# Kernel optimization log

Hardware: AMD Instinct MI355X
Metric: run time of the kernel (lower is better)

Reference implementation:

```python
import jax, jax.numpy as jnp
import numpy as np

B, N, D, H = 4, 2048, 256, 4
DH = D // H          # 64
SCALE = DH ** (-0.5)
LN_EPS = 1e-5


def setup_inputs() -> dict:
    key = jax.random.key(0)
    ks = jax.random.split(key, 16)
    g = lambda k, shape, fan_in: jax.random.normal(k, shape, jnp.float32) / np.sqrt(fan_in)
    # Weights stored as [in, out] (pre-transposed vs torch Linear)
    return {
        "x0": jax.random.normal(ks[0], (B, N, D), jnp.float32),
        "x1": jax.random.normal(ks[1], (B, N, D), jnp.float32),
        "Wqk": g(ks[2], (D, D), D), "bqk": jnp.zeros((D,), jnp.float32),
        "Wv": g(ks[3], (D, D), D), "bv": jnp.zeros((D,), jnp.float32),
        "Wout": g(ks[4], (D, D), D), "bout": jnp.zeros((D,), jnp.float32),
        "Wf1": g(ks[5], (2 * D, 2 * D), 2 * D), "bf1": jnp.zeros((2 * D,), jnp.float32),
        "ln_g": jnp.ones((2 * D,), jnp.float32), "ln_b": jnp.zeros((2 * D,), jnp.float32),
        "Wf2": g(ks[6], (2 * D, D), 2 * D), "bf2": jnp.zeros((D,), jnp.float32),
    }


def _split_heads(t):
    # [B,N,D] -> [B,H,N,DH]
    b, n, _ = t.shape
    return t.reshape(b, n, H, DH).transpose(0, 2, 1, 3)


def _merge_heads(t):
    # [B,H,N,DH] -> [B,N,D]
    b, h, n, dh = t.shape
    return t.transpose(0, 2, 1, 3).reshape(b, n, h * dh)


def _layernorm(x, g, b):
    mu = jnp.mean(x, axis=-1, keepdims=True)
    var = jnp.mean(jnp.square(x - mu), axis=-1, keepdims=True)
    return (x - mu) * jax.lax.rsqrt(var + LN_EPS) * g + b


def reference(x0, x1, Wqk, bqk, Wv, bv, Wout, bout, Wf1, bf1, ln_g, ln_b, Wf2, bf2):
    qk0 = _split_heads(x0 @ Wqk + bqk)   # [B,H,N,DH]
    qk1 = _split_heads(x1 @ Wqk + bqk)
    v0 = _split_heads(x0 @ Wv + bv)
    v1 = _split_heads(x1 @ Wv + bv)

    ss = SCALE ** 0.5
    sim = jnp.einsum('bhid,bhjd->bhij', qk0 * ss, qk1 * ss)  # shared score matrix
    attn01 = jax.nn.softmax(sim, axis=-1)   # normalize over j
    attn10 = jax.nn.softmax(sim, axis=-2)   # normalize over i (== softmax(sim^T) transposed)
    m0 = jnp.einsum('bhij,bhjd->bhid', attn01, v1)
    m1 = jnp.einsum('bhji,bhjd->bhid', attn10, v0)

    m0 = _merge_heads(m0) @ Wout + bout   # [B,N,D]
    m1 = _merge_heads(m1) @ Wout + bout

    def ffn(x):
        h = x @ Wf1 + bf1                 # [B,N,2D]
        h = jax.nn.gelu(_layernorm(h, ln_g, ln_b), approximate=False)
        return h @ Wf2 + bf2              # [B,N,D]

    y0 = x0 + ffn(jnp.concatenate([x0, m0], axis=-1))
    y1 = x1 + ffn(jnp.concatenate([x1, m1], axis=-1))
    return (y0, y1)
```

## Files before the change

kernel.cpp:

```cpp
#include <hip/hip_runtime.h>
#include <hip/hip_bf16.h>
#include <math.h>

typedef __bf16 bf16;
typedef __attribute__((ext_vector_type(8))) __bf16 bf16x8;
typedef __attribute__((ext_vector_type(4))) __bf16 bf16x4;
typedef __attribute__((ext_vector_type(2))) __bf16 bf16x2;
typedef __attribute__((ext_vector_type(4))) float f32x4;
typedef __attribute__((ext_vector_type(16))) float f32x16;
typedef __attribute__((ext_vector_type(4))) unsigned u32x4;

#define MFMA(a,b,c)   __builtin_amdgcn_mfma_f32_16x16x32_bf16(a,b,c,0,0,0)
#define MFMA32(a,b,c) __builtin_amdgcn_mfma_f32_32x32x16_bf16(a,b,c,0,0,0)

static constexpr int Bb = 4, Nn = 2048, Hh = 4;
static constexpr float SS2 = 0.4246609001440095f;

__device__ __forceinline__ void lds16(const bf16* src, bf16* dst) {
  __builtin_amdgcn_global_load_lds(
      (const __attribute__((address_space(1))) void*)src,
      (__attribute__((address_space(3))) void*)dst, 16, 0, 0);
}

__device__ __forceinline__ f32x16 zero16() {
  f32x16 t;
#pragma unroll
  for (int i = 0; i < 16; ++i) t[i] = 0.f;
  return t;
}

__global__ __launch_bounds__(256) void prep_k(
    const float* Wqk, const float* Wv, const float* Wout, const float* bout,
    const float* Wf1, const float* Wf2, const float* x0, const float* x1,
    bf16* wqkv_t, bf16* wout_b, bf16* wfold_t, bf16* wf1b_t, bf16* wf2_t,
    bf16* xb0, bf16* xb1) {
  int id = blockIdx.x * 256 + threadIdx.x;
  if (id < 65536) { int k = id >> 8, n = id & 255; wqkv_t[n*256 + k] = (bf16)Wqk[id]; return; }
  id -= 65536;
  if (id < 65536) { int k = id >> 8, n = id & 255; wqkv_t[(256 + n)*256 + k] = (bf16)Wv[id]; return; }
  id -= 65536;
  if (id < 98304) {
    if (id < 65536) { wout_b[id] = (bf16)Wout[id]; }
    else { int id3 = id - 65536; int r = id3 >> 8, k = id3 & 255;
           wout_b[(256 + r)*256 + k] = (r == 0) ? (bf16)bout[k] : (bf16)0.f; }
    return; }
  id -= 98304;
  if (id < 131072) { int o = id & 511, k = id >> 9; wfold_t[o*512 + k] = (bf16)Wf1[k*512 + o]; return; }
  id -= 131072;
  if (id < 131072) { int o = id & 511, k = id >> 9; wf1b_t[o*256 + k] = (bf16)Wf1[(256 + k)*512 + o]; return; }
  id -= 131072;
  if (id < 131072) { int k = id >> 8, n = id & 255; wf2_t[n*512 + k] = (bf16)Wf2[id]; return; }
  id -= 131072;
  if (id < 1048576) {
    const float* xs = (id < 524288) ? x0 : x1;
    bf16* xd = (id < 524288) ? xb0 : xb1;
    int j = (id < 524288) ? id : id - 524288;
    f32x4 v = *reinterpret_cast<const f32x4*>(&xs[(size_t)j * 4]);
    bf16x4 o; o[0] = (bf16)v[0]; o[1] = (bf16)v[1]; o[2] = (bf16)v[2]; o[3] = (bf16)v[3];
    *reinterpret_cast<bf16x4*>(&xd[(size_t)j * 4]) = o;
  }
}

__global__ __launch_bounds__(256, 2) void qkvfold_k(
    const bf16* xb0, const bf16* xb1, const bf16* wqkv_t,
    const float* bqk, const float* bv,
    bf16* qks0, bf16* qks1, bf16* vT0, bf16* vT1,
    const bf16* wout_b, const bf16* wf1b_t, const float* bf1,
    bf16* wfold_t, float* bfold) {
  const int fid = blockIdx.x;
  const bool fold = fid >= 512;
  int bx, by, bz;
  if (!fold) {
    bx = ((fid & 7) << 3) + ((fid >> 3) & 7);
    by = (fid >> 6) & 3;
    bz = fid >> 8;
  } else {
    int id = fid - 512;
    bx = id % 3; by = id / 3; bz = 0;
  }

  const bf16* Aa = fold ? wout_b : (bz ? xb1 : xb0);
  const bf16* Wt = fold ? wf1b_t : wqkv_t;

  const int tid = threadIdx.x;
  const int lane = tid & 63;
  const int w = tid >> 6;
  const int wr = w >> 1, wc = w & 1;
  const int m0r = bx * 128;
  const int n0 = by * 128;
  const int r15 = lane & 15, g = lane >> 4, rb = r15 & 7;
  const int l3 = lane >> 3, l7 = lane & 7;
  const int swzc = (l7 ^ l3) * 8;

  __shared__ bf16 At[2][8192];
  __shared__ bf16 Bt[2][8192];

  const bf16* aA = Aa + (size_t)(m0r + w*32 + l3) * 256 + swzc;
  const bf16* bB = Wt + (size_t)(n0 + w*32 + l3) * 256 + swzc;
  const int adst = (w*32) * 64;

  auto stage = [&](int buf, int kc) {
#pragma unroll
    for (int i = 0; i < 4; i++)
      lds16(aA + kc*64 + (size_t)i * 8 * 256, &At[buf][adst + i*512]);
#pragma unroll
    for (int i = 0; i < 4; i++)
      lds16(bB + kc*64 + (size_t)i * 8 * 256, &Bt[buf][adst + i*512]);
  };

  f32x4 acc[4][4];
#pragma unroll
  for (int i = 0; i < 4; i++)
#pragma unroll
    for (int j = 0; j < 4; j++) acc[i][j] = f32x4{0.f, 0.f, 0.f, 0.f};

  const int rx0 = ((0*4 + g) ^ rb) << 4;
  const int rx1 = ((1*4 + g) ^ rb) << 4;

  auto compute = [&](int cur) {
    const char* Ap = (const char*)&At[cur][0];
    const char* Bp = (const char*)&Bt[cur][0];
    __builtin_amdgcn_s_setprio(1);
#pragma unroll
    for (int ks = 0; ks < 2; ++ks) {
      const int rx = ks ? rx1 : rx0;
      bf16x8 af[4], bfr[4];
#pragma unroll
      for (int mf = 0; mf < 4; ++mf)
        af[mf] = *reinterpret_cast<const bf16x8*>(Ap + (wr*64 + mf*16 + r15) * 128 + rx);
#pragma unroll
      for (int nf = 0; nf < 4; ++nf)
        bfr[nf] = *reinterpret_cast<const bf16x8*>(Bp + (wc*64 + nf*16 + r15) * 128 + rx);
#pragma unroll
      for (int mf = 0; mf < 4; ++mf)
#pragma unroll
        for (int nf = 0; nf < 4; ++nf)
          acc[mf][nf] = MFMA(af[mf], bfr[nf], acc[mf][nf]);
    }
    __builtin_amdgcn_s_setprio(0);
  };

  stage(0, 0);
  int cur = 0;
  for (int kc = 0; kc < 3; ++kc) {
    stage(cur ^ 1, kc + 1);
    asm volatile("s_waitcnt vmcnt(8)" ::: "memory");
    __builtin_amdgcn_sched_barrier(0);
    __builtin_amdgcn_s_barrier();
    __builtin_amdgcn_sched_barrier(0);
    compute(cur);
    asm volatile("s_waitcnt lgkmcnt(0)" ::: "memory");
    __builtin_amdgcn_sched_barrier(0);
    __builtin_amdgcn_s_barrier();
    __builtin_amdgcn_sched_barrier(0);
    cur ^= 1;
  }
  asm volatile("s_waitcnt vmcnt(0)" ::: "memory");
  __builtin_amdgcn_sched_barrier(0);
  __builtin_amdgcn_s_barrier();
  __builtin_amdgcn_sched_barrier(0);
  compute(cur);

  if (!fold) {
    bf16* qks = bz ? qks1 : qks0;
    bf16* vT  = bz ? vT1  : vT0;
#pragma unroll
    for (int mf = 0; mf < 4; ++mf)
#pragma unroll
      for (int nf = 0; nf < 4; ++nf) {
        f32x4 c = acc[mf][nf];
        int cg = n0 + wc*64 + nf*16 + r15;
#pragma unroll
        for (int r = 0; r < 4; ++r) {
          int rg = m0r + wr*64 + mf*16 + g*4 + r;
          int b = rg >> 11, n = rg & 2047;
          if (cg < 256) {
            float val = (c[r] + bqk[cg]) * SS2;
            int h = cg >> 6, dh = cg & 63;
            qks[(((size_t)(b*Hh + h)) * Nn + n) * 64 + dh] = (bf16)val;
          } else {
            int c2 = cg - 256;
            float val = c[r] + bv[c2];
            int h = c2 >> 6, dh = c2 & 63;
            vT[(((size_t)(b*Hh + h)) * 64 + dh) * Nn + n] = (bf16)val;
          }
        }
      }
  } else {
#pragma unroll
    for (int mf = 0; mf < 4; ++mf)
#pragma unroll
      for (int nf = 0; nf < 4; ++nf) {
        f32x4 c = acc[mf][nf];
        int cg = n0 + wc*64 + nf*16 + r15;
#pragma unroll
        for (int r = 0; r < 4; ++r) {
          int rg = m0r + wr*64 + mf*16 + g*4 + r;
          if (rg < 256) wfold_t[(size_t)cg * 512 + 256 + rg] = (bf16)c[r];
          else if (rg == 256) bfold[cg] = c[r] + bf1[cg];
        }
      }
  }
}

template<int MODE, int BN, int MINW, int REMAP>
__global__ __launch_bounds__(256, MINW) void gemm_k(
    const bf16* Aa0, const bf16* Aa1, const bf16* Ac0, const bf16* Ac1,
    const bf16* Wt, const float* bias,
    bf16* ob0, bf16* ob1, float* of0, float* of1) {
  constexpr int KD  = 512;
  constexpr int LDA = (MODE == 4) ? 512 : 256;
  constexpr int NKC = KD / 64;
  constexpr int NF  = BN / 32;

  int bx = blockIdx.x, by = blockIdx.y, bz = blockIdx.z;
  if constexpr (REMAP == 1) {
    int id = blockIdx.x + 64 * (blockIdx.y + 4 * blockIdx.z);
    bx = ((id & 7) << 3) + ((id >> 3) & 7);
    by = (id >> 6) & 3;
    bz = id >> 8;
  }

  const bf16* Aa = bz ? Aa1 : Aa0;
  const bf16* Ac = bz ? Ac1 : Ac0;
  bf16*  ob = bz ? ob1 : ob0;
  float* of = bz ? of1 : of0;

  const int tid = threadIdx.x;
  const int lane = tid & 63;
  const int w = tid >> 6;
  const int wr = w >> 1, wc = w & 1;
  const int m0r = bx * 128;
  const int n0 = by * BN;
  const int r15 = lane & 15, g = lane >> 4, rb = r15 & 7;
  const int l3 = lane >> 3, l7 = lane & 7;
  const int swzc = (l7 ^ l3) * 8;

  __shared__ bf16 At[2][8192];
  __shared__ bf16 Bt[2][BN * 64];

  const bf16* aA = Aa + (size_t)(m0r + w*32 + l3) * LDA + swzc;
  const bf16* aC = (MODE == 3) ? (Ac + (size_t)(m0r + w*32 + l3) * 256 + swzc) : nullptr;
  const bf16* bB = Wt + (size_t)(n0 + w*(BN/4) + l3) * KD + swzc;
  const int adst = (w*32) * 64;
  const int bdst = (w*(BN/4)) * 64;

  auto stage = [&](int buf, int kc) {
    const bf16* ab; int kcol;
    if constexpr (MODE == 3) {
      if (kc < 4) { ab = aA; kcol = kc * 64; } else { ab = aC; kcol = (kc - 4) * 64; }
    } else { ab = aA; kcol = kc * 64; }
#pragma unroll
    for (int i = 0; i < 4; i++)
      lds16(ab + kcol + (size_t)i * 8 * LDA, &At[buf][adst + i*512]);
#pragma unroll
    for (int i = 0; i < NF; i++)
      lds16(bB + kc*64 + (size_t)i * 8 * KD, &Bt[buf][bdst + i*512]);
  };

  f32x4 acc[4][NF];
#pragma unroll
  for (int i = 0; i < 4; i++)
#pragma unroll
    for (int j = 0; j < NF; j++) acc[i][j] = f32x4{0.f, 0.f, 0.f, 0.f};

  const int rx0 = ((0*4 + g) ^ rb) << 4;
  const int rx1 = ((1*4 + g) ^ rb) << 4;

  auto compute = [&](int cur) {
    const char* Ap = (const char*)&At[cur][0];
    const char* Bp = (const char*)&Bt[cur][0];
    __builtin_amdgcn_s_setprio(1);
#pragma unroll
    for (int ks = 0; ks < 2; ++ks) {
      const int rx = ks ? rx1 : rx0;
      bf16x8 af[4], bfr[NF];
#pragma unroll
      for (int mf = 0; mf < 4; ++mf)
        af[mf] = *reinterpret_cast<const bf16x8*>(Ap + (wr*64 + mf*16 + r15) * 128 + rx);
#pragma unroll
      for (int nf = 0; nf < NF; ++nf)
        bfr[nf] = *reinterpret_cast<const bf16x8*>(Bp + (wc*(BN/2) + nf*16 + r15) * 128 + rx);
#pragma unroll
      for (int mf = 0; mf < 4; ++mf)
#pragma unroll
        for (int nf = 0; nf < NF; ++nf)
          acc[mf][nf] = MFMA(af[mf], bfr[nf], acc[mf][nf]);
    }
    __builtin_amdgcn_s_setprio(0);
  };

  stage(0, 0);
  int cur = 0;
  for (int kc = 0; kc < NKC - 1; ++kc) {
    stage(cur ^ 1, kc + 1);
    if constexpr (NF == 4) asm volatile("s_waitcnt vmcnt(8)" ::: "memory");
    else                   asm volatile("s_waitcnt vmcnt(6)" ::: "memory");
    __builtin_amdgcn_sched_barrier(0);
    __builtin_amdgcn_s_barrier();
    __builtin_amdgcn_sched_barrier(0);
    compute(cur);
    asm volatile("s_waitcnt lgkmcnt(0)" ::: "memory");
    __builtin_amdgcn_sched_barrier(0);
    __builtin_amdgcn_s_barrier();
    __builtin_amdgcn_sched_barrier(0);
    cur ^= 1;
  }
  asm volatile("s_waitcnt vmcnt(0)" ::: "memory");
  __builtin_amdgcn_sched_barrier(0);
  __builtin_amdgcn_s_barrier();
  __builtin_amdgcn_sched_barrier(0);
  compute(cur);

#pragma unroll
  for (int mf = 0; mf < 4; ++mf)
#pragma unroll
    for (int nf = 0; nf < NF; ++nf) {
      f32x4 c = acc[mf][nf];
      int cg = n0 + wc*(BN/2) + nf*16 + r15;
#pragma unroll
      for (int r = 0; r < 4; ++r) {
        int rg = m0r + wr*64 + mf*16 + g*4 + r;
        if constexpr (MODE == 3) {
          ob[(size_t)rg * 512 + cg] = (bf16)(c[r] + bias[cg]);
        } else {
          of[(size_t)rg * 256 + cg] = c[r] + bias[cg] + (float)Ac[(size_t)rg * 256 + cg];
        }
      }
    }
}

__global__ __launch_bounds__(512, 4) void attn_k(
    const bf16* qks0, const bf16* qks1, const bf16* vT0, const bf16* vT1,
    bf16* m0o, bf16* m1o) {
  const int B = blockIdx.x + 16 * (blockIdx.y + 16 * blockIdx.z);
  const int xcd = B & 7, kk = B >> 3;
  const int group = 4 * xcd + (kk >> 4);
  const int it = kk & 15;
  const int bh = group & 15, dir = group >> 4;

  const bf16* Q  = (dir ? qks1 : qks0) + (size_t)bh * (Nn * 64);
  const bf16* Kp = (dir ? qks0 : qks1) + (size_t)bh * (Nn * 64);
  const bf16* Vp = (dir ? vT0  : vT1 ) + (size_t)bh * (64 * Nn);
  bf16* out = dir ? m1o : m0o;
  const int b = bh >> 2, h = bh & 3;

  const int tid = threadIdx.x, lane = tid & 63, w = tid >> 6;
  const int ig = w >> 1, hj = w & 1;
  const int l31 = lane & 31, hi = lane >> 5, xr = l31 & 7;
  const int iw = it * 128 + ig * 32;

  __shared__ char smem[65536];
  bf16* KV = (bf16*)smem;
  const int kbase = hj * 8192;
  const int vbase = 16384 + hj * 8192;

  bf16x8 qf[4];
#pragma unroll
  for (int kt = 0; kt < 4; ++kt)
    qf[kt] = *reinterpret_cast<const bf16x8*>(
        &Q[(size_t)(iw + l31) * 64 + kt*16 + hi*8]);

  bf16x8 ones;
#pragma unroll
  for (int i = 0; i < 8; ++i) ones[i] = (bf16)1.0f;

  f32x16 acc[2]; acc[0] = zero16(); acc[1] = zero16();
  f32x16 rsacc = zero16();

  const int l3 = lane >> 3, l7 = lane & 7;
  const int swz = ((l7 ^ l3) * 8);
  const bf16* ks0 = Kp + (size_t)(ig*16 +     l3) * 64 + swz;
  const bf16* ks1 = Kp + (size_t)(ig*16 + 8 + l3) * 64 + swz;
  const bf16* vs0 = Vp + (size_t)(ig*16 +     l3) * 2048 + swz;
  const bf16* vs1 = Vp + (size_t)(ig*16 + 8 + l3) * 2048 + swz;
  const int kd0 = (ig*16    ) * 64;
  const int kd1 = (ig*16 + 8) * 64;

  auto stage = [&](int buf, int j0) {
    lds16(ks0 + (size_t)j0 * 64, KV + kbase + buf*4096 + kd0);
    lds16(ks1 + (size_t)j0 * 64, KV + kbase + buf*4096 + kd1);
    lds16(vs0 + j0,              KV + vbase + buf*4096 + kd0);
    lds16(vs1 + j0,              KV + vbase + buf*4096 + kd1);
  };

  int kby[2][4], vby[2][4];
#pragma unroll
  for (int jm = 0; jm < 2; ++jm)
#pragma unroll
    for (int kt = 0; kt < 4; ++kt)
      kby[jm][kt] = (jm*32 + l31) * 128 + (((2*kt + hi) ^ xr) << 4);
#pragma unroll
  for (int nt = 0; nt < 2; ++nt)
#pragma unroll
    for (int gg = 0; gg < 4; ++gg)
      vby[nt][gg] = (nt*32 + l31) * 128 + (((2*gg + hi) ^ xr) << 4);

  auto compute_tile = [&](int cur) {
    const char* Kb = (const char*)(KV + kbase + cur*4096);
    const char* Vb = (const char*)(KV + vbase + cur*4096);
    f32x16 st[2];
    __builtin_amdgcn_s_setprio(1);
#pragma unroll
    for (int jm = 0; jm < 2; ++jm) {
      f32x16 t = zero16();
#pragma unroll
      for (int kt = 0; kt < 4; ++kt) {
        bf16x8 kf = *reinterpret_cast<const bf16x8*>(Kb + kby[jm][kt]);
        t = MFMA32(kf, qf[kt], t);
      }
      st[jm] = t;
    }
    __builtin_amdgcn_s_setprio(0);
    bf16x8 pa[4];
#pragma unroll
    for (int jm = 0; jm < 2; ++jm) {
      unsigned dw[8];
#pragma unroll
      for (int s = 0; s < 8; ++s) {
        float e0 = __builtin_amdgcn_exp2f(st[jm][2*s]);
        float e1 = __builtin_amdgcn_exp2f(st[jm][2*s + 1]);
        asm("v_cvt_pk_bf16_f32 %0, %1, %2" : "=v"(dw[s]) : "v"(e0), "v"(e1));
      }
#pragma unroll
      for (int kt2 = 0; kt2 < 2; ++kt2) {
        unsigned a0 = dw[4*kt2 + 0], b0 = dw[4*kt2 + 2];
        unsigned a1 = dw[4*kt2 + 1], b1 = dw[4*kt2 + 3];
        asm volatile("v_permlane32_swap_b32 %0, %1" : "+v"(a0), "+v"(b0));
        asm volatile("v_permlane32_swap_b32 %0, %1" : "+v"(a1), "+v"(b1));
        u32x4 uu; uu[0] = a0; uu[1] = a1; uu[2] = b0; uu[3] = b1;
        pa[jm*2 + kt2] = __builtin_bit_cast(bf16x8, uu);
      }
    }
    __builtin_amdgcn_s_setprio(1);
#pragma unroll
    for (int gg = 0; gg < 4; ++gg) {
      rsacc = MFMA32(pa[gg], ones, rsacc);
#pragma unroll
      for (int nt = 0; nt < 2; ++nt) {
        bf16x8 vf = *reinterpret_cast<const bf16x8*>(Vb + vby[nt][gg]);
        acc[nt] = MFMA32(pa[gg], vf, acc[nt]);
      }
    }
    __builtin_amdgcn_s_setprio(0);
  };

  const int jt0 = hj << 4;
  stage(0, jt0 << 6);
  int cur = 0;
  for (int t = 0; t < 15; ++t) {
    stage(cur ^ 1, (jt0 + t + 1) << 6);
    asm volatile("s_waitcnt vmcnt(4)" ::: "memory");
    __builtin_amdgcn_sched_barrier(0);
    __builtin_amdgcn_s_barrier();
    __builtin_amdgcn_sched_barrier(0);
    compute_tile(cur);
    asm volatile("s_waitcnt lgkmcnt(0)" ::: "memory");
    __builtin_amdgcn_sched_barrier(0);
    __builtin_amdgcn_s_barrier();
    __builtin_amdgcn_sched_barrier(0);
    cur ^= 1;
  }
  asm volatile("s_waitcnt vmcnt(0)" ::: "memory");
  __builtin_amdgcn_sched_barrier(0);
  __builtin_amdgcn_s_barrier();
  __builtin_amdgcn_sched_barrier(0);
  compute_tile(cur);

  __syncthreads();
  float* Ex = (float*)smem;
  if (hj == 1) {
#pragma unroll
    for (int nt = 0; nt < 2; ++nt)
#pragma unroll
      for (int r = 0; r < 16; ++r)
        Ex[(ig*48 + nt*16 + r) * 64 + lane] = acc[nt][r];
#pragma unroll
    for (int r = 0; r < 16; ++r)
      Ex[(ig*48 + 32 + r) * 64 + lane] = rsacc[r];
  }
  __syncthreads();
  if (hj == 0) {
#pragma unroll
    for (int r = 0; r < 16; ++r) {
      float rs = rsacc[r] + Ex[(ig*48 + 32 + r) * 64 + lane];
      float inv = 1.0f / rs;
      int row = iw + (r & 3) + 8*(r >> 2) + 4*hi;
#pragma unroll
      for (int nt = 0; nt < 2; ++nt) {
        float o = acc[nt][r] + Ex[(ig*48 + nt*16 + r) * 64 + lane];
        int col = h*64 + nt*32 + l31;
        out[((size_t)b * Nn + row) * 256 + col] = (bf16)(o * inv);
      }
    }
  }
}

__global__ __launch_bounds__(256) void ln_gelu_k(
    bf16* hg, const float* g, const float* bb) {
  const int row = (blockIdx.x << 2) + (threadIdx.x >> 6);
  const int lane = threadIdx.x & 63;
  bf16* hr = hg + (size_t)row * 512 + lane * 8;
  bf16x8 v = *reinterpret_cast<const bf16x8*>(hr);
  float f[8];
  float s = 0.f, sq = 0.f;
#pragma unroll
  for (int i = 0; i < 8; ++i) { f[i] = (float)v[i]; s += f[i]; sq += f[i]*f[i]; }
#pragma unroll
  for (int m = 1; m < 64; m <<= 1) { s += __shfl_xor(s, m); sq += __shfl_xor(sq, m); }
  float mu = s * (1.f / 512.f);
  float var = sq * (1.f / 512.f) - mu * mu;
  float rsv = rsqrtf(var + 1e-5f);
  f32x4 g0 = *reinterpret_cast<const f32x4*>(&g[lane*8]);
  f32x4 g1 = *reinterpret_cast<const f32x4*>(&g[lane*8 + 4]);
  f32x4 b0 = *reinterpret_cast<const f32x4*>(&bb[lane*8]);
  f32x4 b1 = *reinterpret_cast<const f32x4*>(&bb[lane*8 + 4]);
  bf16x8 o;
#pragma unroll
  for (int i = 0; i < 8; ++i) {
    float gv = (i < 4) ? g0[i] : g1[i-4];
    float bv = (i < 4) ? b0[i] : b1[i-4];
    float xn = (f[i] - mu) * rsv * gv + bv;
    float ge = 0.5f * xn * (1.f + erff(xn * 0.70710678118f));
    o[i] = (bf16)ge;
  }
  *reinterpret_cast<bf16x8*>(hr) = o;
}

extern "C" void kernel_launch(void* const* d_in, const int* in_sizes, int n_in,
                              void* d_out, int out_size, void* d_ws, size_t ws_size,
                              hipStream_t stream) {
  (void)in_sizes; (void)n_in; (void)out_size; (void)ws_size;
  const float* x0   = (const float*)d_in[0];
  const float* x1   = (const float*)d_in[1];
  const float* Wqk  = (const float*)d_in[2];
  const float* bqk  = (const float*)d_in[3];
  const float* Wv   = (const float*)d_in[4];
  const float* bv   = (const float*)d_in[5];
  const float* Wout = (const float*)d_in[6];
  const float* bout = (const float*)d_in[7];
  const float* Wf1  = (const float*)d_in[8];
  const float* bf1  = (const float*)d_in[9];
  const float* ln_g = (const float*)d_in[10];
  const float* ln_b = (const float*)d_in[11];
  const float* Wf2  = (const float*)d_in[12];
  const float* bf2  = (const float*)d_in[13];
  float* y = (float*)d_out;

  bf16* p = (bf16*)d_ws;
  bf16* wqkv_t = p; p += 131072;
  bf16* wout_b = p; p += 98304;
  bf16* wfold_t = p; p += 262144;
  bf16* wf1b_t = p; p += 131072;
  bf16* wf2_t  = p; p += 131072;
  float* bfold = (float*)p; p += 1024;
  bf16* xb0  = p; p += 2097152;
  bf16* xb1  = p; p += 2097152;
  bf16* qks0 = p; p += 2097152;
  bf16* qks1 = p; p += 2097152;
  bf16* vT0  = p; p += 2097152;
  bf16* vT1  = p; p += 2097152;
  bf16* m0   = p; p += 2097152;
  bf16* m1   = p; p += 2097152;
  bf16* hg0  = p; p += 4194304;
  bf16* hg1  = p; p += 4194304;

  dim3 blk(256);
  prep_k<<<6528, blk, 0, stream>>>(Wqk, Wv, Wout, bout, Wf1, Wf2, x0, x1,
                                   wqkv_t, wout_b, wfold_t, wf1b_t, wf2_t, xb0, xb1);
  qkvfold_k<<<dim3(524), blk, 0, stream>>>(
      xb0, xb1, wqkv_t, bqk, bv, qks0, qks1, vT0, vT1,
      wout_b, wf1b_t, bf1, wfold_t, bfold);
  attn_k<<<dim3(16, 16, 2), dim3(512), 0, stream>>>(qks0, qks1, vT0, vT1, m0, m1);
  gemm_k<3,128,2,1><<<dim3(64, 4, 2), blk, 0, stream>>>(
      xb0, xb1, m0, m1, wfold_t, bfold,
      hg0, hg1, nullptr, nullptr);
  ln_gelu_k<<<dim3(4096), blk, 0, stream>>>(hg0, ln_g, ln_b);
  gemm_k<4,64,3,0><<<dim3(64, 4, 2), blk, 0, stream>>>(
      hg0, hg1, xb0, xb1, wf2_t, bf2,
      nullptr, nullptr, y, y + 2097152);
}
```

Measured before the change: 121.5 us.

## Fuse LayerNorm+GELU into FFN GEMMs via partial row statistics

Removes the standalone ln_gelu kernel. The first FFN GEMM now emits per-row partial sums and sums of squares for each column tile into a workspace, and the second GEMM combines them into mean and rstd. The second GEMM then applies LayerNorm and erf-GELU while loading A tiles through registers into LDS. This saves one launch and a full read-write pass over the 2D-wide hidden tensor. In exchange, the second GEMM recomputes GELU for each of its 4 column blocks, loses the async global-to-LDS loads for A, and waits with vmcnt(0) every iteration, which weakens overlap.

Result: slower. 142.3 us (+17.1%).

```diff
diff --git a/kernel.cpp b/kernel.cpp
--- a/kernel.cpp
+++ b/kernel.cpp
@@ -203,28 +203,20 @@
   }
 }
 
-template<int MODE, int BN, int MINW, int REMAP>
-__global__ __launch_bounds__(256, MINW) void gemm_k(
+__global__ __launch_bounds__(256, 2) void gemm3_k(
     const bf16* Aa0, const bf16* Aa1, const bf16* Ac0, const bf16* Ac1,
     const bf16* Wt, const float* bias,
-    bf16* ob0, bf16* ob1, float* of0, float* of1) {
-  constexpr int KD  = 512;
-  constexpr int LDA = (MODE == 4) ? 512 : 256;
-  constexpr int NKC = KD / 64;
-  constexpr int NF  = BN / 32;
-
-  int bx = blockIdx.x, by = blockIdx.y, bz = blockIdx.z;
-  if constexpr (REMAP == 1) {
-    int id = blockIdx.x + 64 * (blockIdx.y + 4 * blockIdx.z);
-    bx = ((id & 7) << 3) + ((id >> 3) & 7);
-    by = (id >> 6) & 3;
-    bz = id >> 8;
-  }
+    bf16* ob0, bf16* ob1, float* part) {
+  constexpr int KD = 512, LDA = 256, NKC = 8, NF = 4, BN = 128;
+
+  int id = blockIdx.x + 64 * (blockIdx.y + 4 * blockIdx.z);
+  int bx = ((id & 7) << 3) + ((id >> 3) & 7);
+  int by = (id >> 6) & 3;
+  int bz = id >> 8;
 
   const bf16* Aa = bz ? Aa1 : Aa0;
   const bf16* Ac = bz ? Ac1 : Ac0;
-  bf16*  ob = bz ? ob1 : ob0;
-  float* of = bz ? of1 : of0;
+  bf16* ob = bz ? ob1 : ob0;
 
   const int tid = threadIdx.x;
   const int lane = tid & 63;
@@ -240,16 +232,14 @@
   __shared__ bf16 Bt[2][BN * 64];
 
   const bf16* aA = Aa + (size_t)(m0r + w*32 + l3) * LDA + swzc;
-  const bf16* aC = (MODE == 3) ? (Ac + (size_t)(m0r + w*32 + l3) * 256 + swzc) : nullptr;
+  const bf16* aC = Ac + (size_t)(m0r + w*32 + l3) * 256 + swzc;
   const bf16* bB = Wt + (size_t)(n0 + w*(BN/4) + l3) * KD + swzc;
   const int adst = (w*32) * 64;
   const int bdst = (w*(BN/4)) * 64;
 
   auto stage = [&](int buf, int kc) {
     const bf16* ab; int kcol;
-    if constexpr (MODE == 3) {
-      if (kc < 4) { ab = aA; kcol = kc * 64; } else { ab = aC; kcol = (kc - 4) * 64; }
-    } else { ab = aA; kcol = kc * 64; }
+    if (kc < 4) { ab = aA; kcol = kc * 64; } else { ab = aC; kcol = (kc - 4) * 64; }
 #pragma unroll
     for (int i = 0; i < 4; i++)
       lds16(ab + kcol + (size_t)i * 8 * LDA, &At[buf][adst + i*512]);
@@ -294,8 +284,7 @@
   int cur = 0;
   for (int kc = 0; kc < NKC - 1; ++kc) {
     stage(cur ^ 1, kc + 1);
-    if constexpr (NF == 4) asm volatile("s_waitcnt vmcnt(8)" ::: "memory");
-    else                   asm volatile("s_waitcnt vmcnt(6)" ::: "memory");
+    asm volatile("s_waitcnt vmcnt(8)" ::: "memory");
     __builtin_amdgcn_sched_barrier(0);
     __builtin_amdgcn_s_barrier();
     __builtin_amdgcn_sched_barrier(0);
@@ -312,20 +301,211 @@
   __builtin_amdgcn_sched_barrier(0);
   compute(cur);
 
+  float s_[4][4], s2_[4][4];
+#pragma unroll
+  for (int mf = 0; mf < 4; ++mf)
+#pragma unroll
+    for (int r = 0; r < 4; ++r) { s_[mf][r] = 0.f; s2_[mf][r] = 0.f; }
 #pragma unroll
   for (int mf = 0; mf < 4; ++mf)
 #pragma unroll
     for (int nf = 0; nf < NF; ++nf) {
       f32x4 c = acc[mf][nf];
       int cg = n0 + wc*(BN/2) + nf*16 + r15;
+      float bch = bias[cg];
 #pragma unroll
       for (int r = 0; r < 4; ++r) {
         int rg = m0r + wr*64 + mf*16 + g*4 + r;
-        if constexpr (MODE == 3) {
-          ob[(size_t)rg * 512 + cg] = (bf16)(c[r] + bias[cg]);
-        } else {
-          of[(size_t)rg * 256 + cg] = c[r] + bias[cg] + (float)Ac[(size_t)rg * 256 + cg];
-        }
+        float val = c[r] + bch;
+        ob[(size_t)rg * 512 + cg] = (bf16)val;
+        s_[mf][r] += val; s2_[mf][r] += val * val;
+      }
+    }
+#pragma unroll
+  for (int mf = 0; mf < 4; ++mf)
+#pragma unroll
+    for (int r = 0; r < 4; ++r) {
+#pragma unroll
+      for (int m = 1; m < 16; m <<= 1) {
+        s_[mf][r]  += __shfl_xor(s_[mf][r],  m);
+        s2_[mf][r] += __shfl_xor(s2_[mf][r], m);
+      }
+    }
+  asm volatile("s_waitcnt lgkmcnt(0)" ::: "memory");
+  __syncthreads();
+  float* sred = (float*)&At[0][0];
+  if (r15 == 0) {
+#pragma unroll
+    for (int mf = 0; mf < 4; ++mf)
+#pragma unroll
+      for (int r = 0; r < 4; ++r) {
+        int row = wr*64 + mf*16 + g*4 + r;
+        sred[(wc*128 + row)*2    ] = s_[mf][r];
+        sred[(wc*128 + row)*2 + 1] = s2_[mf][r];
+      }
+  }
+  __syncthreads();
+  if (tid < 128) {
+    int row = tid;
+    float S  = sred[row*2]     + sred[(128+row)*2];
+    float S2 = sred[row*2 + 1] + sred[(128+row)*2 + 1];
+    size_t R = (size_t)bz*8192 + m0r + row;
+    *reinterpret_cast<float2*>(&part[((size_t)by*16384 + R)*2]) = float2{S, S2};
+  }
+}
+
+__global__ __launch_bounds__(256, 2) void ffn2_k(
+    const bf16* Aa0, const bf16* Aa1, const bf16* Ac0, const bf16* Ac1,
+    const bf16* Wt, const float* bias,
+    float* of0, float* of1,
+    const float* lng, const float* lnb, const float* part) {
+  constexpr int KD = 512, LDA = 512, NKC = 8, NF = 2, BN = 64;
+
+  const int bx = blockIdx.x, by = blockIdx.y, bz = blockIdx.z;
+  const bf16* Aa = bz ? Aa1 : Aa0;
+  const bf16* Ac = bz ? Ac1 : Ac0;
+  float* of = bz ? of1 : of0;
+
+  const int tid = threadIdx.x;
+  const int lane = tid & 63;
+  const int w = tid >> 6;
+  const int wr = w >> 1, wc = w & 1;
+  const int m0r = bx * 128;
+  const int n0 = by * BN;
+  const int r15 = lane & 15, g = lane >> 4, rb = r15 & 7;
+  const int l3 = lane >> 3, l7 = lane & 7;
+  const int swzc = (l7 ^ l3) * 8;
+
+  __shared__ bf16 At[2][8192];
+  __shared__ bf16 Bt[2][4096];
+  __shared__ float gld[512], bld[512];
+  __shared__ float rstat[128][2];
+
+  for (int i = tid; i < 512; i += 256) { gld[i] = lng[i]; bld[i] = lnb[i]; }
+  if (tid < 128) {
+    size_t R = (size_t)bz * 8192 + m0r + tid;
+    float S = 0.f, S2 = 0.f;
+#pragma unroll
+    for (int q = 0; q < 4; ++q) {
+      float2 pq = *reinterpret_cast<const float2*>(&part[((size_t)q*16384 + R)*2]);
+      S += pq.x; S2 += pq.y;
+    }
+    float mu = S * (1.f / 512.f);
+    float var = S2 * (1.f / 512.f) - mu * mu;
+    rstat[tid][0] = mu;
+    rstat[tid][1] = rsqrtf(var + 1e-5f);
+  }
+  __syncthreads();
+
+  const bf16* aA = Aa + (size_t)(m0r + w*32 + l3) * LDA + swzc;
+  const bf16* bB = Wt + (size_t)(n0 + w*16 + l3) * KD + swzc;
+  const int adst = (w*32) * 64;
+  const int bdst = (w*16) * 64;
+
+  float mu_[4], rs_[4];
+#pragma unroll
+  for (int i = 0; i < 4; ++i) {
+    int rowl = w*32 + i*8 + l3;
+    mu_[i] = rstat[rowl][0];
+    rs_[i] = rstat[rowl][1];
+  }
+
+  auto loadA = [&](int kc, bf16x8* ar) {
+#pragma unroll
+    for (int i = 0; i < 4; ++i)
+      ar[i] = *reinterpret_cast<const bf16x8*>(aA + kc*64 + (size_t)i * 8 * LDA);
+  };
+  auto writeA = [&](int buf, const bf16x8* ar, int kc) {
+    const int cb = kc*64 + swzc;
+    f32x4 gv0 = *reinterpret_cast<const f32x4*>(&gld[cb]);
+    f32x4 gv1 = *reinterpret_cast<const f32x4*>(&gld[cb + 4]);
+    f32x4 bv0 = *reinterpret_cast<const f32x4*>(&bld[cb]);
+    f32x4 bv1 = *reinterpret_cast<const f32x4*>(&bld[cb + 4]);
+#pragma unroll
+    for (int i = 0; i < 4; ++i) {
+      bf16x8 o;
+#pragma unroll
+      for (int j = 0; j < 8; ++j) {
+        float f = (float)ar[i][j];
+        float gv = (j < 4) ? gv0[j] : gv1[j - 4];
+        float bv = (j < 4) ? bv0[j] : bv1[j - 4];
+        float xn = (f - mu_[i]) * rs_[i] * gv + bv;
+        float ge = 0.5f * xn * (1.f + erff(xn * 0.70710678118f));
+        o[j] = (bf16)ge;
+      }
+      *reinterpret_cast<bf16x8*>(&At[buf][adst + i*512 + lane*8]) = o;
+    }
+  };
+  auto stageB = [&](int buf, int kc) {
+#pragma unroll
+    for (int i = 0; i < NF; i++)
+      lds16(bB + kc*64 + (size_t)i * 8 * KD, &Bt[buf][bdst + i*512]);
+  };
+
+  f32x4 acc[4][NF];
+#pragma unroll
+  for (int i = 0; i < 4; i++)
+#pragma unroll
+    for (int j = 0; j < NF; j++) acc[i][j] = f32x4{0.f, 0.f, 0.f, 0.f};
+
+  const int rx0 = ((0*4 + g) ^ rb) << 4;
+  const int rx1 = ((1*4 + g) ^ rb) << 4;
+
+  auto compute = [&](int cur) {
+    const char* Ap = (const char*)&At[cur][0];
+    const char* Bp = (const char*)&Bt[cur][0];
+    __builtin_amdgcn_s_setprio(1);
+#pragma unroll
+    for (int ks = 0; ks < 2; ++ks) {
+      const int rx = ks ? rx1 : rx0;
+      bf16x8 af[4], bfr[NF];
+#pragma unroll
+      for (int mf = 0; mf < 4; ++mf)
+        af[mf] = *reinterpret_cast<const bf16x8*>(Ap + (wr*64 + mf*16 + r15) * 128 + rx);
+#pragma unroll
+      for (int nf = 0; nf < NF; ++nf)
+        bfr[nf] = *reinterpret_cast<const bf16x8*>(Bp + (wc*32 + nf*16 + r15) * 128 + rx);
+#pragma unroll
+      for (int mf = 0; mf < 4; ++mf)
+#pragma unroll
+        for (int nf = 0; nf < NF; ++nf)
+          acc[mf][nf] = MFMA(af[mf], bfr[nf], acc[mf][nf]);
+    }
+    __builtin_amdgcn_s_setprio(0);
+  };
+
+  bf16x8 ar[4];
+  loadA(0, ar);
+  stageB(0, 0);
+  writeA(0, ar, 0);
+  asm volatile("s_waitcnt vmcnt(0) lgkmcnt(0)" ::: "memory");
+  __builtin_amdgcn_sched_barrier(0);
+  __builtin_amdgcn_s_barrier();
+  __builtin_amdgcn_sched_barrier(0);
+  int cur = 0;
+  for (int kc = 0; kc < NKC - 1; ++kc) {
+    loadA(kc + 1, ar);
+    stageB(cur ^ 1, kc + 1);
+    compute(cur);
+    writeA(cur ^ 1, ar, kc + 1);
+    asm volatile("s_waitcnt vmcnt(0) lgkmcnt(0)" ::: "memory");
+    __builtin_amdgcn_sched_barrier(0);
+    __builtin_amdgcn_s_barrier();
+    __builtin_amdgcn_sched_barrier(0);
+    cur ^= 1;
+  }
+  compute(cur);
+
+#pragma unroll
+  for (int mf = 0; mf < 4; ++mf)
+#pragma unroll
+    for (int nf = 0; nf < NF; ++nf) {
+      f32x4 c = acc[mf][nf];
+      int cg = n0 + wc*32 + nf*16 + r15;
+#pragma unroll
+      for (int r = 0; r < 4; ++r) {
+        int rg = m0r + wr*64 + mf*16 + g*4 + r;
+        of[(size_t)rg * 256 + cg] = c[r] + bias[cg] + (float)Ac[(size_t)rg * 256 + cg];
       }
     }
 }
@@ -494,37 +674,6 @@
       }
     }
   }
-}
-
-__global__ __launch_bounds__(256) void ln_gelu_k(
-    bf16* hg, const float* g, const float* bb) {
-  const int row = (blockIdx.x << 2) + (threadIdx.x >> 6);
-  const int lane = threadIdx.x & 63;
-  bf16* hr = hg + (size_t)row * 512 + lane * 8;
-  bf16x8 v = *reinterpret_cast<const bf16x8*>(hr);
-  float f[8];
-  float s = 0.f, sq = 0.f;
-#pragma unroll
-  for (int i = 0; i < 8; ++i) { f[i] = (float)v[i]; s += f[i]; sq += f[i]*f[i]; }
-#pragma unroll
-  for (int m = 1; m < 64; m <<= 1) { s += __shfl_xor(s, m); sq += __shfl_xor(sq, m); }
-  float mu = s * (1.f / 512.f);
-  float var = sq * (1.f / 512.f) - mu * mu;
-  float rsv = rsqrtf(var + 1e-5f);
-  f32x4 g0 = *reinterpret_cast<const f32x4*>(&g[lane*8]);
-  f32x4 g1 = *reinterpret_cast<const f32x4*>(&g[lane*8 + 4]);
-  f32x4 b0 = *reinterpret_cast<const f32x4*>(&bb[lane*8]);
-  f32x4 b1 = *reinterpret_cast<const f32x4*>(&bb[lane*8 + 4]);
-  bf16x8 o;
-#pragma unroll
-  for (int i = 0; i < 8; ++i) {
-    float gv = (i < 4) ? g0[i] : g1[i-4];
-    float bv = (i < 4) ? b0[i] : b1[i-4];
-    float xn = (f[i] - mu) * rsv * gv + bv;
-    float ge = 0.5f * xn * (1.f + erff(xn * 0.70710678118f));
-    o[i] = (bf16)ge;
-  }
-  *reinterpret_cast<bf16x8*>(hr) = o;
 }
 
 extern "C" void kernel_launch(void* const* d_in, const int* in_sizes, int n_in,
@@ -554,6 +703,7 @@
   bf16* wf1b_t = p; p += 131072;
   bf16* wf2_t  = p; p += 131072;
   float* bfold = (float*)p; p += 1024;
+  float* part  = (float*)p; p += 262144;
   bf16* xb0  = p; p += 2097152;
   bf16* xb1  = p; p += 2097152;
   bf16* qks0 = p; p += 2097152;
@@ -572,11 +722,9 @@
       xb0, xb1, wqkv_t, bqk, bv, qks0, qks1, vT0, vT1,
       wout_b, wf1b_t, bf1, wfold_t, bfold);
   attn_k<<<dim3(16, 16, 2), dim3(512), 0, stream>>>(qks0, qks1, vT0, vT1, m0, m1);
-  gemm_k<3,128,2,1><<<dim3(64, 4, 2), blk, 0, stream>>>(
-      xb0, xb1, m0, m1, wfold_t, bfold,
-      hg0, hg1, nullptr, nullptr);
-  ln_gelu_k<<<dim3(4096), blk, 0, stream>>>(hg0, ln_g, ln_b);
-  gemm_k<4,64,3,0><<<dim3(64, 4, 2), blk, 0, stream>>>(
+  gemm3_k<<<dim3(64, 4, 2), blk, 0, stream>>>(
+      xb0, xb1, m0, m1, wfold_t, bfold, hg0, hg1, part);
+  ffn2_k<<<dim3(64, 4, 2), blk, 0, stream>>>(
       hg0, hg1, xb0, xb1, wf2_t, bf2,
-      nullptr, nullptr, y, y + 2097152);
+      y, y + 2097152, ln_g, ln_b, part);
 }
```
